# Performance work log

Hardware: AMD Instinct MI355X
Metric: run time of the kernel (lower is better)

Reference implementation:

```python
import jax, jax.numpy as jnp
import numpy as np
from jax import lax

FEATURE_NUM = 16
FILTERS = 64
BATCH = 64
WINDOW = 5
T = 2048
SECTORS = 11
D = 256          # embedding dim / number of quantization buckets
DA = 64
VOCAB = 100000
L = T - 3 * WINDOW + 3  # 2036, length after conv->maxpool->conv (all valid, stride 1)
BN_EPS = 1e-5


def _conv1d(x, w):
    # x: [N, C, W], w: [O, I, K], valid padding, stride 1
    return lax.conv_general_dilated(x, w, (1,), 'VALID', dimension_numbers=('NCH', 'OIH', 'NCH'))


def setup_inputs() -> dict:
    key = jax.random.key(0)
    ks = jax.random.split(key, 9)
    x = jax.random.normal(ks[0], (BATCH, 2 * FEATURE_NUM, T), jnp.float32)
    conv1_w = jax.random.normal(ks[1], (FILTERS, 2 * FEATURE_NUM, WINDOW), jnp.float32) * 0.1
    conv1_b = jnp.zeros((FILTERS,), jnp.float32)
    bn_gamma = jnp.ones((FILTERS,), jnp.float32)
    bn_beta = jnp.zeros((FILTERS,), jnp.float32)
    conv2_w = jax.random.normal(ks[2], (1, FILTERS, WINDOW), jnp.float32) * 0.1
    conv2_b = jnp.zeros((1,), jnp.float32)
    emb = jax.random.normal(ks[3], (VOCAB, D), jnp.float32)
    W1 = jax.random.normal(ks[4], (DA, L), jnp.float32)
    W2 = jax.random.normal(ks[5], (DA, 1), jnp.float32)
    lin_w = jax.random.normal(ks[6], (SECTORS, D), jnp.float32) * 0.05
    lin_b = jnp.zeros((SECTORS,), jnp.float32)
    return {'x': x, 'conv1_w': conv1_w, 'conv1_b': conv1_b, 'bn_gamma': bn_gamma,
            'bn_beta': bn_beta, 'conv2_w': conv2_w, 'conv2_b': conv2_b, 'emb': emb,
            'W1': W1, 'W2': W2, 'lin_w': lin_w, 'lin_b': lin_b}


def reference(x, conv1_w, conv1_b, bn_gamma, bn_beta, conv2_w, conv2_b, emb, W1, W2, lin_w, lin_b):
    # conv1 (valid) -> maxpool(k=WINDOW, s=1) -> batchnorm (train-mode batch stats) -> conv2 -> relu
    h = _conv1d(x, conv1_w) + conv1_b[None, :, None]                     # [B, F, T-W+1]
    h = lax.reduce_window(h, -jnp.inf, lax.max, (1, 1, WINDOW), (1, 1, 1), 'VALID')
    mu = jnp.mean(h, axis=(0, 2), keepdims=True)
    var = jnp.mean((h - mu) ** 2, axis=(0, 2), keepdims=True)            # biased, as torch BN train
    h = (h - mu) * lax.rsqrt(var + BN_EPS) * bn_gamma[None, :, None] + bn_beta[None, :, None]
    h = jax.nn.relu(_conv1d(h, conv2_w) + conv2_b[None, :, None])        # [B, 1, L]
    c = jax.nn.sigmoid(h[:, 0, :])                                       # [B, L] in (0,1)
    # embedding_generate: first j with c <= (j+1)/D  <=>  j = ceil(c*D) - 1
    idx = jnp.clip(jnp.ceil(c * D).astype(jnp.int32) - 1, 0, D - 1)      # [B, L]
    e = emb[idx]                                                         # [B, L, D]
    # per-sample attention: A = W2^T tanh(W1 @ out), batched as einsums
    t = jnp.tanh(jnp.einsum('al,bld->bad', W1, e))                       # [B, DA, D]
    A = jnp.einsum('a,bad->bd', W2[:, 0], t)                             # [B, D]
    att = jax.nn.softmax(jnp.einsum('bld,bd->bl', e, A), axis=1)         # [B, L]
    scores = A @ lin_w.T + lin_b                                         # [B, SECTORS]
    return att, scores
```

## Files before the change

kernel.cpp:

```cpp
#include <hip/hip_runtime.h>
#include <hip/hip_bf16.h>
#include <math.h>

#define BATCH 64
#define CIN   32
#define TIN   2048
#define FILT  64
#define WIN   5
#define TP1   2044
#define TP2   2040
#define LOUT  2036
#define DEMB  256
#define DA    64
#define NSEC  11
#define NC    4
#define CS    509
#define CT_TILE 504

__global__ __launch_bounds__(256) void k_prep(
    const float* __restrict__ W1, const float* __restrict__ emb,
    const float* __restrict__ w1, float* __restrict__ w1t,
    float* __restrict__ embT, float* __restrict__ w1r, int* __restrict__ count) {
  __shared__ float tl[64 * 65];
  int bk = blockIdx.x;
  const int tid = threadIdx.x;
  if (bk < 64) { count[bk * 256 + tid] = 0; return; }
  bk -= 64;
  if (bk < 32) {
    const int l0 = bk * 64;
    const int lc = tid & 63, rq = tid >> 6;
    for (int a = rq; a < 64; a += 4)
      tl[a * 65 + lc] = (l0 + lc < LOUT) ? W1[a * LOUT + l0 + lc] : 0.f;
    __syncthreads();
    for (int lp = rq; lp < 64; lp += 4)
      if (l0 + lp < LOUT) w1t[(l0 + lp) * 64 + lc] = tl[lc * 65 + lp];
    return;
  }
  bk -= 32;
  if (bk < 16) {
    const int j0 = (bk & 3) * 64, d0 = (bk >> 2) * 64;
    const int c = tid & 63, rq = tid >> 6;
    for (int j = rq; j < 64; j += 4) tl[j * 65 + c] = emb[(j0 + j) * DEMB + d0 + c];
    __syncthreads();
    for (int d = rq; d < 64; d += 4) embT[(d0 + d) * DEMB + j0 + c] = tl[c * 65 + d];
    return;
  }
  bk -= 16;
  {
    int i = bk * 256 + tid;
    int c = i / 320, r = i - c * 320, f = r / 5, k = r - f * 5;
    w1r[i] = w1[f * (CIN * WIN) + c * WIN + k];
  }
}

__global__ __launch_bounds__(256) void k_conv1pool(
    const float* __restrict__ x, const float* __restrict__ w1r,
    const float* __restrict__ b1, float* __restrict__ h2) {
  __shared__ float wl[CIN * 80];
  const int b   = blockIdx.y;
  const int t0  = blockIdx.x * CT_TILE;
  const int tid = threadIdx.x;
  const int z   = blockIdx.z;

  for (int i = tid; i < CIN * 80; i += 256) {
    int c = i >> 6 >> 1 ? 0 : 0, cc = i / 80, r = i - cc * 80;
    (void)c;
    wl[i] = w1r[cc * 320 + z * 80 + r];
  }
  __syncthreads();

  const int tg   = tid & 63;
  const int tb   = tg * 8;
  const int wv20 = (tid >> 6) * 20;
  const int wf0  = __builtin_amdgcn_readfirstlane(z * 16 + (tid >> 6) * 4);

  float acc[4][8];
#pragma unroll
  for (int ff = 0; ff < 4; ++ff) {
    float bias = b1[wf0 + ff];
#pragma unroll
    for (int j = 0; j < 8; ++j) acc[ff][j] = bias;
  }

  const float* xrow = x + (size_t)b * CIN * TIN + t0 + tb;
  const bool safe = (t0 + tb + 12) <= TIN;

  for (int c = 0; c < CIN; ++c) {
    float xw[12];
    if (safe) {
      float4 a0 = *(const float4*)(xrow + c * TIN);
      float4 a1 = *(const float4*)(xrow + c * TIN + 4);
      float4 a2 = *(const float4*)(xrow + c * TIN + 8);
      xw[0] = a0.x; xw[1] = a0.y; xw[2]  = a0.z; xw[3]  = a0.w;
      xw[4] = a1.x; xw[5] = a1.y; xw[6]  = a1.z; xw[7]  = a1.w;
      xw[8] = a2.x; xw[9] = a2.y; xw[10] = a2.z; xw[11] = a2.w;
    } else {
#pragma unroll
      for (int j = 0; j < 12; ++j) {
        int gt = t0 + tb + j;
        xw[j] = (gt < TIN) ? xrow[c * TIN + j] : 0.f;
      }
    }
#pragma unroll
    for (int q = 0; q < 5; ++q) {
      float4 wq = *(const float4*)&wl[c * 80 + wv20 + q * 4];
      float wv[4] = {wq.x, wq.y, wq.z, wq.w};
#pragma unroll
      for (int r = 0; r < 4; ++r) {
        const int wi = q * 4 + r;
        const int ff = wi / 5, k = wi % 5;
#pragma unroll
        for (int j = 0; j < 8; ++j)
          acc[ff][j] = fmaf(xw[k + j], wv[r], acc[ff][j]);
      }
    }
  }

  const bool lanevalid = (tg < 63);
#pragma unroll
  for (int ff = 0; ff < 4; ++ff) {
    float n0 = __shfl_down(acc[ff][0], 1);
    float n1 = __shfl_down(acc[ff][1], 1);
    float n2 = __shfl_down(acc[ff][2], 1);
    float n3 = __shfl_down(acc[ff][3], 1);
    float h[12] = {acc[ff][0], acc[ff][1], acc[ff][2], acc[ff][3],
                   acc[ff][4], acc[ff][5], acc[ff][6], acc[ff][7],
                   n0, n1, n2, n3};
    float o[8];
#pragma unroll
    for (int j = 0; j < 8; ++j) {
      float m = fmaxf(fmaxf(h[j], h[j + 1]), fmaxf(h[j + 2], h[j + 3]));
      o[j] = fmaxf(m, h[j + 4]);
    }
    const int f = wf0 + ff;
    const int t2b = t0 + tb;
    if (lanevalid && (t2b + 7 < TP2)) {
      float* dst = &h2[((size_t)b * FILT + f) * TP2 + t2b];
      *(float4*)dst = make_float4(o[0], o[1], o[2], o[3]);
      *(float4*)(dst + 4) = make_float4(o[4], o[5], o[6], o[7]);
    } else if (lanevalid) {
#pragma unroll
      for (int j = 0; j < 8; ++j) {
        int t2 = t2b + j;
        if (t2 < TP2) h2[((size_t)b * FILT + f) * TP2 + t2] = o[j];
      }
    }
  }
}

__global__ __launch_bounds__(256) void k_bnstat(
    const float* __restrict__ h2, double* __restrict__ bn_s,
    double* __restrict__ bn_q) {
  const int g = blockIdx.x, f = blockIdx.y;
  const int tid = threadIdx.x;
  double s = 0.0, q = 0.0;
  for (int bl = 0; bl < 8; ++bl) {
    const float* row = h2 + ((size_t)(g * 8 + bl) * FILT + f) * TP2;
    for (int i = tid; i < 510; i += 256) {
      float4 v = *(const float4*)(row + i * 4);
      s += (double)v.x + (double)v.y + (double)v.z + (double)v.w;
      q += (double)v.x * v.x + (double)v.y * v.y +
           (double)v.z * v.z + (double)v.w * v.w;
    }
  }
#pragma unroll
  for (int off = 32; off > 0; off >>= 1) {
    s += __shfl_down(s, off);
    q += __shfl_down(q, off);
  }
  __shared__ double lsd[4], lqd[4];
  if ((tid & 63) == 0) { lsd[tid >> 6] = s; lqd[tid >> 6] = q; }
  __syncthreads();
  if (tid == 0) {
    bn_s[f * 8 + g] = lsd[0] + lsd[1] + lsd[2] + lsd[3];
    bn_q[f * 8 + g] = lqd[0] + lqd[1] + lqd[2] + lqd[3];
  }
}

__global__ __launch_bounds__(256) void k_conv2(
    const float* __restrict__ h2, const double* __restrict__ bn_s,
    const double* __restrict__ bn_q, const float* __restrict__ gamma,
    const float* __restrict__ beta, const float* __restrict__ w2,
    const float* __restrict__ b2, int* __restrict__ idxp,
    int* __restrict__ count) {
  __shared__ float hl[FILT * 260];
  __shared__ int hist[DEMB];
  __shared__ double ws2l[FILT * WIN];
  __shared__ double c0l;
  const int b = blockIdx.y;
  const int t0 = blockIdx.x * 256;
  const int tid = threadIdx.x;

  if (tid < 64) {
    double s = 0.0, q = 0.0;
#pragma unroll
    for (int g = 0; g < 8; ++g) { s += bn_s[tid * 8 + g]; q += bn_q[tid * 8 + g]; }
    const double N = (double)(BATCH * TP2);
    double mu  = s / N;
    double var = q / N - mu * mu;
    double sc  = (double)gamma[tid] / sqrt(var + 1e-5);
    double sh  = (double)beta[tid] - mu * sc;
    double wsum = 0.0;
#pragma unroll
    for (int k = 0; k < WIN; ++k) {
      double wv = (double)w2[tid * WIN + k];
      ws2l[tid * WIN + k] = sc * wv;
      wsum += wv;
    }
    double part = sh * wsum;
#pragma unroll
    for (int off = 32; off > 0; off >>= 1) part += __shfl_down(part, off);
    if (tid == 0) c0l = part + (double)b2[0];
  }
  for (int i = tid; i < FILT * 260; i += 256) {
    int f = i / 260, o = i - f * 260;
    int gt = t0 + o;
    hl[i] = (gt < TP2) ? h2[((size_t)b * FILT + f) * TP2 + gt] : 0.f;
  }
  hist[tid] = 0;
  __syncthreads();
  const int t = t0 + tid;
  if (t < LOUT) {
    double z = c0l;
    for (int f = 0; f < FILT; ++f) {
      const double* wr = &ws2l[f * WIN];
      z = fma((double)hl[f * 260 + tid + 0], wr[0], z);
      z = fma((double)hl[f * 260 + tid + 1], wr[1], z);
      z = fma((double)hl[f * 260 + tid + 2], wr[2], z);
      z = fma((double)hl[f * 260 + tid + 3], wr[3], z);
      z = fma((double)hl[f * 260 + tid + 4], wr[4], z);
    }
    z = z > 0.0 ? z : 0.0;
    double c = 1.0 / (1.0 + exp(-z));
    int iv = (int)ceil(c * 256.0) - 1;
    iv = min(max(iv, 0), DEMB - 1);
    idxp[b * LOUT + t] = iv;
    atomicAdd(&hist[iv], 1);
  }
  __syncthreads();
  atomicAdd(&count[b * DEMB + tid], hist[tid]);
}

__global__ __launch_bounds__(256) void k_sbuild(
    const int* __restrict__ idxp, const float* __restrict__ w1t,
    float* __restrict__ Sg) {
  __shared__ float S[DA * 257];
  __shared__ int il[512];
  const int b = blockIdx.y, ch = blockIdx.x;
  const int tid = threadIdx.x;
  for (int i = tid; i < DA * 257; i += 256) S[i] = 0.f;
  const int l0 = ch * CS;
  for (int i = tid; i < CS; i += 256) il[i] = idxp[b * LOUT + l0 + i];
  __syncthreads();
  const int a = tid & 63, w = tid >> 6;
#pragma unroll 4
  for (int li = w; li < CS; li += 4) {
    int j = il[li];
    float v = w1t[(l0 + li) * DA + a];
    atomicAdd(&S[a * 257 + j], v);
  }
  __syncthreads();
  for (int i = tid; i < DA * DEMB; i += 256) {
    int aa = i >> 8, j = i & 255;
    Sg[((b * NC + ch) * DA + aa) * DEMB + j] = S[aa * 257 + j];
  }
}

__global__ __launch_bounds__(256) void k_gemmA(
    const float* __restrict__ Sg, const float* __restrict__ emb,
    const float* __restrict__ W2, float* __restrict__ Avec) {
  __shared__ float Al[16 * 64];
  __shared__ float Bl[16 * 64];
  __shared__ float red[16 * 64];
  const int b = blockIdx.x, c0 = blockIdx.y * 64;
  const int tid = threadIdx.x;
  const int tx = tid & 15, ty = tid >> 4;
  const int sa = tid >> 2, skq = (tid & 3) * 4;
  const int bk = tid >> 4, bseg = tid & 15;
  float acc[4][4] = {{0}};

  for (int kc = 0; kc < 16; ++kc) {
    const int kb = kc * 16;
    float4 v0 = *(const float4*)&Sg[((b * NC + 0) * DA + sa) * DEMB + kb + skq];
    float4 v1 = *(const float4*)&Sg[((b * NC + 1) * DA + sa) * DEMB + kb + skq];
    float4 v2 = *(const float4*)&Sg[((b * NC + 2) * DA + sa) * DEMB + kb + skq];
    float4 v3 = *(const float4*)&Sg[((b * NC + 3) * DA + sa) * DEMB + kb + skq];
    float4 sv = make_float4(v0.x + v1.x + v2.x + v3.x, v0.y + v1.y + v2.y + v3.y,
                            v0.z + v1.z + v2.z + v3.z, v0.w + v1.w + v2.w + v3.w);
    Al[(skq + 0) * 64 + sa] = sv.x;
    Al[(skq + 1) * 64 + sa] = sv.y;
    Al[(skq + 2) * 64 + sa] = sv.z;
    Al[(skq + 3) * 64 + sa] = sv.w;
    float4 e4 = *(const float4*)&emb[(kb + bk) * DEMB + c0 + bseg * 4];
    *(float4*)&Bl[bk * 64 + bseg * 4] = e4;
    __syncthreads();
#pragma unroll
    for (int k = 0; k < 16; ++k) {
      float4 av = *(const float4*)&Al[k * 64 + ty * 4];
      float4 bv = *(const float4*)&Bl[k * 64 + tx * 4];
      acc[0][0] = fmaf(av.x, bv.x, acc[0][0]); acc[0][1] = fmaf(av.x, bv.y, acc[0][1]);
      acc[0][2] = fmaf(av.x, bv.z, acc[0][2]); acc[0][3] = fmaf(av.x, bv.w, acc[0][3]);
      acc[1][0] = fmaf(av.y, bv.x, acc[1][0]); acc[1][1] = fmaf(av.y, bv.y, acc[1][1]);
      acc[1][2] = fmaf(av.y, bv.z, acc[1][2]); acc[1][3] = fmaf(av.y, bv.w, acc[1][3]);
      acc[2][0] = fmaf(av.z, bv.x, acc[2][0]); acc[2][1] = fmaf(av.z, bv.y, acc[2][1]);
      acc[2][2] = fmaf(av.z, bv.z, acc[2][2]); acc[2][3] = fmaf(av.z, bv.w, acc[2][3]);
      acc[3][0] = fmaf(av.w, bv.x, acc[3][0]); acc[3][1] = fmaf(av.w, bv.y, acc[3][1]);
      acc[3][2] = fmaf(av.w, bv.z, acc[3][2]); acc[3][3] = fmaf(av.w, bv.w, acc[3][3]);
    }
    __syncthreads();
  }
  float cs[4] = {0.f, 0.f, 0.f, 0.f};
#pragma unroll
  for (int r = 0; r < 4; ++r) {
    float wv = W2[ty * 4 + r];
#pragma unroll
    for (int j = 0; j < 4; ++j) cs[j] += tanhf(acc[r][j]) * wv;
  }
#pragma unroll
  for (int j = 0; j < 4; ++j) red[ty * 64 + tx * 4 + j] = cs[j];
  __syncthreads();
  if (tid < 64) {
    float s = 0.f;
#pragma unroll
    for (int q = 0; q < 16; ++q) s += red[q * 64 + tid];
    Avec[b * DEMB + c0 + tid] = s;
  }
}

__global__ __launch_bounds__(256) void k_att(
    const float* __restrict__ Avec, const float* __restrict__ embT,
    const int* __restrict__ count, const float* __restrict__ linw,
    const float* __restrict__ linb, const int* __restrict__ idxp,
    float* __restrict__ att, float* __restrict__ scores) {
  __shared__ float Al[DEMB];
  __shared__ float pl[DEMB];
  __shared__ float scratch[4];
  const int b = blockIdx.x, j = threadIdx.x;
  Al[j] = Avec[b * DEMB + j];
  __syncthreads();
  float dot = 0.f;
  for (int d = 0; d < DEMB; ++d) dot = fmaf(embT[d * DEMB + j], Al[d], dot);
  const int cnt = count[b * DEMB + j];
  float v = (cnt > 0) ? dot : -3.4e38f;
#pragma unroll
  for (int off = 32; off > 0; off >>= 1) v = fmaxf(v, __shfl_down(v, off));
  if ((j & 63) == 0) scratch[j >> 6] = v;
  __syncthreads();
  const float m = fmaxf(fmaxf(scratch[0], scratch[1]), fmaxf(scratch[2], scratch[3]));
  __syncthreads();
  float e = (cnt > 0) ? expf(dot - m) : 0.f;
  float zs = e * (float)cnt;
#pragma unroll
  for (int off = 32; off > 0; off >>= 1) zs += __shfl_down(zs, off);
  if ((j & 63) == 0) scratch[j >> 6] = zs;
  __syncthreads();
  const float Z = scratch[0] + scratch[1] + scratch[2] + scratch[3];
  pl[j] = (cnt > 0) ? e / Z : 0.f;
  __syncthreads();
  for (int l = j; l < LOUT; l += 256)
    att[b * LOUT + l] = pl[idxp[b * LOUT + l]];
  const int w = j >> 6, lane = j & 63;
  for (int s = w; s < NSEC; s += 4) {
    float part = 0.f;
#pragma unroll
    for (int r = 0; r < 4; ++r)
      part = fmaf(Al[lane + r * 64], linw[s * DEMB + lane + r * 64], part);
#pragma unroll
    for (int off = 32; off > 0; off >>= 1) part += __shfl_down(part, off);
    if (lane == 0) scores[b * NSEC + s] = part + linb[s];
  }
}

extern "C" void kernel_launch(void* const* d_in, const int* in_sizes, int n_in,
                              void* d_out, int out_size, void* d_ws, size_t ws_size,
                              hipStream_t stream) {
  const float* x      = (const float*)d_in[0];
  const float* w1     = (const float*)d_in[1];
  const float* b1     = (const float*)d_in[2];
  const float* gamma  = (const float*)d_in[3];
  const float* beta   = (const float*)d_in[4];
  const float* w2     = (const float*)d_in[5];
  const float* b2     = (const float*)d_in[6];
  const float* emb    = (const float*)d_in[7];
  const float* W1     = (const float*)d_in[8];
  const float* W2     = (const float*)d_in[9];
  const float* linw   = (const float*)d_in[10];
  const float* linb   = (const float*)d_in[11];

  char* ws = (char*)d_ws;
  int*    count = (int*)   (ws + 0);
  double* bn_s  = (double*)(ws + 65536);
  double* bn_q  = (double*)(ws + 69632);
  int*    idxp  = (int*)   (ws + 73728);
  float*  w1t   = (float*) (ws + 594944);
  float*  embT  = (float*) (ws + 1116160);
  float*  Avec  = (float*) (ws + 1378304);
  float*  w1r   = (float*) (ws + 1443840);
  float*  h2    = (float*) (ws + 1484800);
  float*  Sg    = (float*) (ws + 34908160);

  float* att_out    = (float*)d_out;
  float* scores_out = (float*)d_out + BATCH * LOUT;

  k_prep<<<dim3(152), 256, 0, stream>>>(W1, emb, w1, w1t, embT, w1r, count);
  k_conv1pool<<<dim3(5, 64, 4), 256, 0, stream>>>(x, w1r, b1, h2);
  k_bnstat<<<dim3(8, 64), 256, 0, stream>>>(h2, bn_s, bn_q);
  k_conv2<<<dim3(8, 64), 256, 0, stream>>>(h2, bn_s, bn_q, gamma, beta, w2, b2,
                                           idxp, count);
  k_sbuild<<<dim3(NC, 64), 256, 0, stream>>>(idxp, w1t, Sg);
  k_gemmA<<<dim3(64, 4), 256, 0, stream>>>(Sg, emb, W2, Avec);
  k_att<<<dim3(64), 256, 0, stream>>>(Avec, embT, count, linw, linb, idxp,
                                      att_out, scores_out);
}
```

Baseline: 332.3 us.

## Fuse BN statistics into conv1/pool kernel and prefetch conv1 input rows

Removes the separate batch-norm statistics kernel by having each conv1+maxpool wave reduce its pooled outputs in double and atomically accumulate per-filter sums into global buffers, which k_prep now zeroes. This avoids a full re-read of the h2 activation buffer and one kernel launch. It also software-pipelines the per-channel x loads in conv1, vectorizes the h2 tile loads in conv2, and doubles the thread count of the S-build kernel. Double-precision atomics make the summation order nondeterministic and may contend, since many waves update each of the 64 filters.

```diff
diff --git a/kernel.cpp b/kernel.cpp
--- a/kernel.cpp
+++ b/kernel.cpp
@@ -1,5 +1,4 @@
 #include <hip/hip_runtime.h>
-#include <hip/hip_bf16.h>
 #include <math.h>
 
 #define BATCH 64
@@ -20,11 +19,16 @@
 __global__ __launch_bounds__(256) void k_prep(
     const float* __restrict__ W1, const float* __restrict__ emb,
     const float* __restrict__ w1, float* __restrict__ w1t,
-    float* __restrict__ embT, float* __restrict__ w1r, int* __restrict__ count) {
+    float* __restrict__ embT, float* __restrict__ w1r, int* __restrict__ count,
+    double* __restrict__ bn_s, double* __restrict__ bn_q) {
   __shared__ float tl[64 * 65];
   int bk = blockIdx.x;
   const int tid = threadIdx.x;
-  if (bk < 64) { count[bk * 256 + tid] = 0; return; }
+  if (bk < 64) {
+    count[bk * 256 + tid] = 0;
+    if (bk == 0 && tid < 64) { bn_s[tid] = 0.0; bn_q[tid] = 0.0; }
+    return;
+  }
   bk -= 64;
   if (bk < 32) {
     const int l0 = bk * 64;
@@ -55,7 +59,8 @@
 
 __global__ __launch_bounds__(256) void k_conv1pool(
     const float* __restrict__ x, const float* __restrict__ w1r,
-    const float* __restrict__ b1, float* __restrict__ h2) {
+    const float* __restrict__ b1, float* __restrict__ h2,
+    double* __restrict__ bn_s, double* __restrict__ bn_q) {
   __shared__ float wl[CIN * 80];
   const int b   = blockIdx.y;
   const int t0  = blockIdx.x * CT_TILE;
@@ -63,8 +68,7 @@
   const int z   = blockIdx.z;
 
   for (int i = tid; i < CIN * 80; i += 256) {
-    int c = i >> 6 >> 1 ? 0 : 0, cc = i / 80, r = i - cc * 80;
-    (void)c;
+    int cc = i / 80, r = i - cc * 80;
     wl[i] = w1r[cc * 320 + z * 80 + r];
   }
   __syncthreads();
@@ -85,22 +89,29 @@
   const float* xrow = x + (size_t)b * CIN * TIN + t0 + tb;
   const bool safe = (t0 + tb + 12) <= TIN;
 
-  for (int c = 0; c < CIN; ++c) {
-    float xw[12];
-    if (safe) {
-      float4 a0 = *(const float4*)(xrow + c * TIN);
-      float4 a1 = *(const float4*)(xrow + c * TIN + 4);
-      float4 a2 = *(const float4*)(xrow + c * TIN + 8);
-      xw[0] = a0.x; xw[1] = a0.y; xw[2]  = a0.z; xw[3]  = a0.w;
-      xw[4] = a1.x; xw[5] = a1.y; xw[6]  = a1.z; xw[7]  = a1.w;
-      xw[8] = a2.x; xw[9] = a2.y; xw[10] = a2.z; xw[11] = a2.w;
-    } else {
-#pragma unroll
-      for (int j = 0; j < 12; ++j) {
-        int gt = t0 + tb + j;
-        xw[j] = (gt < TIN) ? xrow[c * TIN + j] : 0.f;
-      }
-    }
+#define LOADC(c, r0, r1, r2)                                         \
+  do {                                                               \
+    const float* xc_ = xrow + (size_t)(c) * TIN;                     \
+    if (safe) {                                                      \
+      r0 = *(const float4*)(xc_);                                    \
+      r1 = *(const float4*)(xc_ + 4);                                \
+      r2 = *(const float4*)(xc_ + 8);                                \
+    } else {                                                         \
+      float t_[12];                                                  \
+      _Pragma("unroll")                                              \
+      for (int j_ = 0; j_ < 12; ++j_) {                              \
+        int gt_ = t0 + tb + j_;                                      \
+        t_[j_] = (gt_ < TIN) ? xc_[j_] : 0.f;                        \
+      }                                                              \
+      r0 = make_float4(t_[0], t_[1], t_[2], t_[3]);                  \
+      r1 = make_float4(t_[4], t_[5], t_[6], t_[7]);                  \
+      r2 = make_float4(t_[8], t_[9], t_[10], t_[11]);                \
+    }                                                                \
+  } while (0)
+
+  auto fma_c = [&](int c, float4 A0, float4 A1, float4 A2) {
+    float xw[12] = {A0.x, A0.y, A0.z, A0.w, A1.x, A1.y, A1.z, A1.w,
+                    A2.x, A2.y, A2.z, A2.w};
 #pragma unroll
     for (int q = 0; q < 5; ++q) {
       float4 wq = *(const float4*)&wl[c * 80 + wv20 + q * 4];
@@ -114,9 +125,22 @@
           acc[ff][j] = fmaf(xw[k + j], wv[r], acc[ff][j]);
       }
     }
-  }
+  };
+
+  float4 p0, p1, p2;
+  LOADC(0, p0, p1, p2);
+#pragma unroll 2
+  for (int c = 0; c < CIN - 1; ++c) {
+    float4 n0, n1, n2;
+    LOADC(c + 1, n0, n1, n2);
+    fma_c(c, p0, p1, p2);
+    p0 = n0; p1 = n1; p2 = n2;
+  }
+  fma_c(CIN - 1, p0, p1, p2);
+#undef LOADC
 
   const bool lanevalid = (tg < 63);
+  const int t2b = t0 + tb;
 #pragma unroll
   for (int ff = 0; ff < 4; ++ff) {
     float n0 = __shfl_down(acc[ff][0], 1);
@@ -133,7 +157,28 @@
       o[j] = fmaxf(m, h[j + 4]);
     }
     const int f = wf0 + ff;
-    const int t2b = t0 + tb;
+
+    double sd = 0.0, qd = 0.0;
+    if (lanevalid) {
+#pragma unroll
+      for (int j = 0; j < 8; ++j) {
+        if (t2b + j < TP2) {
+          double v = (double)o[j];
+          sd += v;
+          qd = fma(v, v, qd);
+        }
+      }
+    }
+#pragma unroll
+    for (int off = 32; off > 0; off >>= 1) {
+      sd += __shfl_down(sd, off);
+      qd += __shfl_down(qd, off);
+    }
+    if (tg == 0) {
+      atomicAdd(&bn_s[f], sd);
+      atomicAdd(&bn_q[f], qd);
+    }
+
     if (lanevalid && (t2b + 7 < TP2)) {
       float* dst = &h2[((size_t)b * FILT + f) * TP2 + t2b];
       *(float4*)dst = make_float4(o[0], o[1], o[2], o[3]);
@@ -145,35 +190,6 @@
         if (t2 < TP2) h2[((size_t)b * FILT + f) * TP2 + t2] = o[j];
       }
     }
-  }
-}
-
-__global__ __launch_bounds__(256) void k_bnstat(
-    const float* __restrict__ h2, double* __restrict__ bn_s,
-    double* __restrict__ bn_q) {
-  const int g = blockIdx.x, f = blockIdx.y;
-  const int tid = threadIdx.x;
-  double s = 0.0, q = 0.0;
-  for (int bl = 0; bl < 8; ++bl) {
-    const float* row = h2 + ((size_t)(g * 8 + bl) * FILT + f) * TP2;
-    for (int i = tid; i < 510; i += 256) {
-      float4 v = *(const float4*)(row + i * 4);
-      s += (double)v.x + (double)v.y + (double)v.z + (double)v.w;
-      q += (double)v.x * v.x + (double)v.y * v.y +
-           (double)v.z * v.z + (double)v.w * v.w;
-    }
-  }
-#pragma unroll
-  for (int off = 32; off > 0; off >>= 1) {
-    s += __shfl_down(s, off);
-    q += __shfl_down(q, off);
-  }
-  __shared__ double lsd[4], lqd[4];
-  if ((tid & 63) == 0) { lsd[tid >> 6] = s; lqd[tid >> 6] = q; }
-  __syncthreads();
-  if (tid == 0) {
-    bn_s[f * 8 + g] = lsd[0] + lsd[1] + lsd[2] + lsd[3];
-    bn_q[f * 8 + g] = lqd[0] + lqd[1] + lqd[2] + lqd[3];
   }
 }
 
@@ -192,9 +208,7 @@
   const int tid = threadIdx.x;
 
   if (tid < 64) {
-    double s = 0.0, q = 0.0;
-#pragma unroll
-    for (int g = 0; g < 8; ++g) { s += bn_s[tid * 8 + g]; q += bn_q[tid * 8 + g]; }
+    double s = bn_s[tid], q = bn_q[tid];
     const double N = (double)(BATCH * TP2);
     double mu  = s / N;
     double var = q / N - mu * mu;
@@ -212,10 +226,17 @@
     for (int off = 32; off > 0; off >>= 1) part += __shfl_down(part, off);
     if (tid == 0) c0l = part + (double)b2[0];
   }
-  for (int i = tid; i < FILT * 260; i += 256) {
-    int f = i / 260, o = i - f * 260;
-    int gt = t0 + o;
-    hl[i] = (gt < TP2) ? h2[((size_t)b * FILT + f) * TP2 + gt] : 0.f;
+  for (int i = tid; i < FILT * 65; i += 256) {
+    int f = i / 65, o4 = (i - f * 65) * 4;
+    int gt = t0 + o4;
+    const float* src = &h2[((size_t)b * FILT + f) * TP2 + gt];
+    if (gt + 3 < TP2) {
+      *(float4*)&hl[f * 260 + o4] = *(const float4*)src;
+    } else {
+#pragma unroll
+      for (int k = 0; k < 4; ++k)
+        hl[f * 260 + o4 + k] = (gt + k < TP2) ? src[k] : 0.f;
+    }
   }
   hist[tid] = 0;
   __syncthreads();
@@ -241,26 +262,26 @@
   atomicAdd(&count[b * DEMB + tid], hist[tid]);
 }
 
-__global__ __launch_bounds__(256) void k_sbuild(
+__global__ __launch_bounds__(512) void k_sbuild(
     const int* __restrict__ idxp, const float* __restrict__ w1t,
     float* __restrict__ Sg) {
   __shared__ float S[DA * 257];
   __shared__ int il[512];
   const int b = blockIdx.y, ch = blockIdx.x;
   const int tid = threadIdx.x;
-  for (int i = tid; i < DA * 257; i += 256) S[i] = 0.f;
+  for (int i = tid; i < DA * 257; i += 512) S[i] = 0.f;
   const int l0 = ch * CS;
-  for (int i = tid; i < CS; i += 256) il[i] = idxp[b * LOUT + l0 + i];
+  for (int i = tid; i < CS; i += 512) il[i] = idxp[b * LOUT + l0 + i];
   __syncthreads();
   const int a = tid & 63, w = tid >> 6;
 #pragma unroll 4
-  for (int li = w; li < CS; li += 4) {
+  for (int li = w; li < CS; li += 8) {
     int j = il[li];
     float v = w1t[(l0 + li) * DA + a];
     atomicAdd(&S[a * 257 + j], v);
   }
   __syncthreads();
-  for (int i = tid; i < DA * DEMB; i += 256) {
+  for (int i = tid; i < DA * DEMB; i += 512) {
     int aa = i >> 8, j = i & 255;
     Sg[((b * NC + ch) * DA + aa) * DEMB + j] = S[aa * 257 + j];
   }
@@ -402,12 +423,12 @@
   float* att_out    = (float*)d_out;
   float* scores_out = (float*)d_out + BATCH * LOUT;
 
-  k_prep<<<dim3(152), 256, 0, stream>>>(W1, emb, w1, w1t, embT, w1r, count);
-  k_conv1pool<<<dim3(5, 64, 4), 256, 0, stream>>>(x, w1r, b1, h2);
-  k_bnstat<<<dim3(8, 64), 256, 0, stream>>>(h2, bn_s, bn_q);
+  k_prep<<<dim3(152), 256, 0, stream>>>(W1, emb, w1, w1t, embT, w1r, count,
+                                        bn_s, bn_q);
+  k_conv1pool<<<dim3(5, 64, 4), 256, 0, stream>>>(x, w1r, b1, h2, bn_s, bn_q);
   k_conv2<<<dim3(8, 64), 256, 0, stream>>>(h2, bn_s, bn_q, gamma, beta, w2, b2,
                                            idxp, count);
-  k_sbuild<<<dim3(NC, 64), 256, 0, stream>>>(idxp, w1t, Sg);
+  k_sbuild<<<dim3(NC, 64), 512, 0, stream>>>(idxp, w1t, Sg);
   k_gemmA<<<dim3(64, 4), 256, 0, stream>>>(Sg, emb, W2, Avec);
   k_att<<<dim3(64), 256, 0, stream>>>(Avec, embT, count, linw, linb, idxp,
                                       att_out, scores_out);
```

Measured after the change: 389.9 us. 17.3% more time.
